# Performance work log

Measured on AMD Instinct MI355X. Metric: run time of the kernel, lower is better.

The kernel has to match this reference:

```python
import jax, jax.numpy as jnp
import numpy as np

L = 6
LVL = 2

def build_permutation_indices(L, l):
    delta = 4 ** (L - l - 1)
    tmp = np.tile(np.arange(4) * delta, delta)
    tmp += np.repeat(np.arange(delta), 4)
    tmp = np.tile(tmp, 4 ** l)
    tmp += np.repeat(np.arange(4 ** l) * 4 ** (L - l), 4 ** (L - l))
    return tmp.astype(np.int32)

def setup_inputs() -> dict:
    key = jax.random.key(0)
    ks = jax.random.split(key, 5)
    B, N, r = 16, 4 ** L, 32
    m, s = N // 4, 4 * r
    glorot = float(np.sqrt(1.0 / s))  # ~glorot scale for (s,s) matmul
    x = jax.random.normal(ks[0], (B, 2, N, r), dtype=jnp.float32)
    hr1 = jax.random.normal(ks[1], (m, s, s), dtype=jnp.float32) * glorot
    hi1 = jax.random.normal(ks[2], (m, s, s), dtype=jnp.float32) * glorot
    hr2 = jax.random.normal(ks[3], (m, s, s), dtype=jnp.float32) * glorot
    hi2 = jax.random.normal(ks[4], (m, s, s), dtype=jnp.float32) * glorot
    perm_idx = jnp.asarray(build_permutation_indices(L, LVL))
    return {"x": x, "hr1": hr1, "hi1": hi1, "hr2": hr2, "hi2": hi2, "perm_idx": perm_idx}

def reference(x, hr1, hi1, hr2, hi2, perm_idx):
    m = x.shape[-2] // 4
    s = x.shape[-1] * 4
    # permutation gather along the row axis, then regroup into m blocks of size s
    xp = jnp.take(x, perm_idx, axis=-2).reshape((-1, 2, m, s))
    x_re, x_im = xp[:, 0, :, :], xp[:, 1, :, :]
    # complex block-diagonal matmul: four real batched GEMMs over blocks 'a'
    y_re = jnp.einsum('baj,ajk->bak', x_re, hr1) + jnp.einsum('baj,ajk->bak', x_im, hi1)
    y_im = jnp.einsum('baj,ajk->bak', x_re, hi2) + jnp.einsum('baj,ajk->bak', x_im, hr2)
    y = jnp.stack([y_re, y_im], axis=1)
    n, r = m * 4, s // 4
    return y.reshape((-1, 2, n, r))
```

## Files before the change

kernel.cpp:

```cpp
#include <hip/hip_runtime.h>


__global__ __launch_bounds__(256, 4)
void hmat_kernel(const float* __restrict__ x,
                 const float* __restrict__ hr1,
                 const float* __restrict__ hi1,
                 const float* __restrict__ hr2,
                 const float* __restrict__ hi2,
                 const int* __restrict__ perm,
                 float* __restrict__ out) {
  __shared__ float lds[4096];
  const int a = blockIdx.x;
  const int t = threadIdx.x;

  {
    const int b    = t >> 4;
    const int c    = (t >> 3) & 1;
    const int jg   = (t >> 1) & 3;
    const int half = t & 1;
    const int row  = perm[a * 4 + jg];
    const float4* src =
        (const float4*)(x + ((size_t)(b * 2 + c) * 4096 + (size_t)row) * 32 +
                        half * 16);
#pragma unroll
    for (int q = 0; q < 4; ++q) {
      const float4 v = src[q];
      const int jb = jg * 32 + half * 16 + q * 4;
      lds[(jb + 0) * 32 + c * 16 + b] = v.x;
      lds[(jb + 1) * 32 + c * 16 + b] = v.y;
      lds[(jb + 2) * 32 + c * 16 + b] = v.z;
      lds[(jb + 3) * 32 + c * 16 + b] = v.w;
    }
  }
  __syncthreads();

  const int w    = t >> 6;
  const int ch   = w >> 1;
  const int jh   = w & 1;
  const int lane = t & 63;
  const int m    = lane >> 5;
  const int kg   = lane & 31;
  const int k0   = kg * 4;

  const float* __restrict__ Hm =
      (ch == 0) ? (m == 0 ? hr1 : hi1) : (m == 0 ? hi2 : hr2);
  const float* __restrict__ hp =
      Hm + (size_t)a * 16384 + (size_t)jh * 8192 + k0;
  const float* __restrict__ xp = lds + jh * 2048 + m * 16;

  float4 acc[16];
#pragma unroll
  for (int i = 0; i < 16; ++i) acc[i] = make_float4(0.f, 0.f, 0.f, 0.f);

  float4 pf0 = *(const float4*)(hp + 0 * 128);
  float4 pf1 = *(const float4*)(hp + 1 * 128);
  float4 pf2 = *(const float4*)(hp + 2 * 128);
  float4 pf3 = *(const float4*)(hp + 3 * 128);

#define CONSUME(PF, J)                                                     \
  {                                                                        \
    const float* xj = xp + (J) * 32;                                       \
    const float4 xa = *(const float4*)(xj + 0);                            \
    const float4 xb = *(const float4*)(xj + 4);                            \
    const float4 xc = *(const float4*)(xj + 8);                            \
    const float4 xd = *(const float4*)(xj + 12);                           \
    const float xs[16] = {xa.x, xa.y, xa.z, xa.w, xb.x, xb.y, xb.z, xb.w,  \
                          xc.x, xc.y, xc.z, xc.w, xd.x, xd.y, xd.z, xd.w}; \
    _Pragma("unroll") for (int bb = 0; bb < 16; ++bb) {                    \
      acc[bb].x = fmaf(xs[bb], (PF).x, acc[bb].x);                         \
      acc[bb].y = fmaf(xs[bb], (PF).y, acc[bb].y);                         \
      acc[bb].z = fmaf(xs[bb], (PF).z, acc[bb].z);                         \
      acc[bb].w = fmaf(xs[bb], (PF).w, acc[bb].w);                         \
    }                                                                      \
  }

  for (int j4 = 0; j4 < 60; j4 += 4) {
    CONSUME(pf0, j4 + 0); pf0 = *(const float4*)(hp + (j4 + 4) * 128);
    CONSUME(pf1, j4 + 1); pf1 = *(const float4*)(hp + (j4 + 5) * 128);
    CONSUME(pf2, j4 + 2); pf2 = *(const float4*)(hp + (j4 + 6) * 128);
    CONSUME(pf3, j4 + 3); pf3 = *(const float4*)(hp + (j4 + 7) * 128);
  }
  CONSUME(pf0, 60);
  CONSUME(pf1, 61);
  CONSUME(pf2, 62);
  CONSUME(pf3, 63);
#undef CONSUME

#pragma unroll
  for (int bb = 0; bb < 16; ++bb) {
    acc[bb].x += __shfl_xor(acc[bb].x, 32, 64);
    acc[bb].y += __shfl_xor(acc[bb].y, 32, 64);
    acc[bb].z += __shfl_xor(acc[bb].z, 32, 64);
    acc[bb].w += __shfl_xor(acc[bb].w, 32, 64);
  }

  __syncthreads();
  if (jh == 1 && m == 0) {
#pragma unroll
    for (int bb = 0; bb < 16; ++bb)
      *(float4*)&lds[ch * 2048 + bb * 128 + k0] = acc[bb];
  }
  __syncthreads();
  if (jh == 0 && m == 0) {
#pragma unroll
    for (int bb = 0; bb < 16; ++bb) {
      const float4 o = *(const float4*)&lds[ch * 2048 + bb * 128 + k0];
      float4 r;
      r.x = acc[bb].x + o.x;
      r.y = acc[bb].y + o.y;
      r.z = acc[bb].z + o.z;
      r.w = acc[bb].w + o.w;
      *(float4*)(out + (size_t)(bb * 2 + ch) * 131072 + (size_t)a * 128 + k0) =
          r;
    }
  }
}

extern "C" void kernel_launch(void* const* d_in, const int* in_sizes, int n_in,
                              void* d_out, int out_size, void* d_ws, size_t ws_size,
                              hipStream_t stream) {
  const float* x   = (const float*)d_in[0];
  const float* hr1 = (const float*)d_in[1];
  const float* hi1 = (const float*)d_in[2];
  const float* hr2 = (const float*)d_in[3];
  const float* hi2 = (const float*)d_in[4];
  const int* perm  = (const int*)d_in[5];
  float* out = (float*)d_out;

  hipLaunchKernelGGL(hmat_kernel, dim3(1024), dim3(256), 0, stream,
                     x, hr1, hi1, hr2, hi2, perm, out);
}
```

Measured before the change: 57.19 us.

## Swizzle LDS x tile, double-buffer LDS reads, and overlap H prefetch with staging

The x staging tile in LDS now uses an XOR swizzle on the column index, which is meant to cut bank conflicts on both the transposing writes and the float4 reads. The first H prefetch loads are issued before the barrier, so their global latency overlaps the x staging. LDS reads of x are double-buffered in registers one step ahead of the FMA block to hide LDS latency. The trade-off is more register pressure under launch_bounds(256,4), plus fiddly swizzle index arithmetic that must match between writes and reads.

```diff
diff --git a/kernel.cpp b/kernel.cpp
--- a/kernel.cpp
+++ b/kernel.cpp
@@ -13,27 +13,6 @@
   const int a = blockIdx.x;
   const int t = threadIdx.x;
 
-  {
-    const int b    = t >> 4;
-    const int c    = (t >> 3) & 1;
-    const int jg   = (t >> 1) & 3;
-    const int half = t & 1;
-    const int row  = perm[a * 4 + jg];
-    const float4* src =
-        (const float4*)(x + ((size_t)(b * 2 + c) * 4096 + (size_t)row) * 32 +
-                        half * 16);
-#pragma unroll
-    for (int q = 0; q < 4; ++q) {
-      const float4 v = src[q];
-      const int jb = jg * 32 + half * 16 + q * 4;
-      lds[(jb + 0) * 32 + c * 16 + b] = v.x;
-      lds[(jb + 1) * 32 + c * 16 + b] = v.y;
-      lds[(jb + 2) * 32 + c * 16 + b] = v.z;
-      lds[(jb + 3) * 32 + c * 16 + b] = v.w;
-    }
-  }
-  __syncthreads();
-
   const int w    = t >> 6;
   const int ch   = w >> 1;
   const int jh   = w & 1;
@@ -46,26 +25,55 @@
       (ch == 0) ? (m == 0 ? hr1 : hi1) : (m == 0 ? hi2 : hr2);
   const float* __restrict__ hp =
       Hm + (size_t)a * 16384 + (size_t)jh * 8192 + k0;
-  const float* __restrict__ xp = lds + jh * 2048 + m * 16;
 
-  float4 acc[16];
-#pragma unroll
-  for (int i = 0; i < 16; ++i) acc[i] = make_float4(0.f, 0.f, 0.f, 0.f);
+  {
+    const int b    = t >> 4;
+    const int c    = (t >> 3) & 1;
+    const int jg   = (t >> 1) & 3;
+    const int half = t & 1;
+    const int row  = perm[a * 4 + jg];
+    const float4* src =
+        (const float4*)(x + ((size_t)(b * 2 + c) * 4096 + (size_t)row) * 32 +
+                        half * 16);
+    float4 v0 = src[0], v1 = src[1], v2 = src[2], v3 = src[3];
+    const int col = (c * 16 + b) ^ ((((jg << 1) | half) & 3) << 2);
+    const int jb  = jg * 32 + half * 16;
+#define PUTX(V, Q)                             \
+  lds[(jb + (Q)*4 + 0) * 32 + col] = (V).x;    \
+  lds[(jb + (Q)*4 + 1) * 32 + col] = (V).y;    \
+  lds[(jb + (Q)*4 + 2) * 32 + col] = (V).z;    \
+  lds[(jb + (Q)*4 + 3) * 32 + col] = (V).w;
+    PUTX(v0, 0) PUTX(v1, 1) PUTX(v2, 2) PUTX(v3, 3)
+#undef PUTX
+  }
 
   float4 pf0 = *(const float4*)(hp + 0 * 128);
   float4 pf1 = *(const float4*)(hp + 1 * 128);
   float4 pf2 = *(const float4*)(hp + 2 * 128);
   float4 pf3 = *(const float4*)(hp + 3 * 128);
 
-#define CONSUME(PF, J)                                                     \
+  __syncthreads();
+
+  const float* __restrict__ xp = lds + m * 16;
+
+  float4 acc[16];
+#pragma unroll
+  for (int i = 0; i < 16; ++i) acc[i] = make_float4(0.f, 0.f, 0.f, 0.f);
+
+#define LOADX(X0, X1, X2, X3, J)                        \
+  {                                                     \
+    const float* xj = xp + (J) * 32;                    \
+    const int key = (((J) >> 4) & 3) << 2;              \
+    X0 = *(const float4*)(xj + (0 ^ key));              \
+    X1 = *(const float4*)(xj + (4 ^ key));              \
+    X2 = *(const float4*)(xj + (8 ^ key));              \
+    X3 = *(const float4*)(xj + (12 ^ key));             \
+  }
+
+#define CONSUME(PF, XA, XB, XC, XD)                                        \
   {                                                                        \
-    const float* xj = xp + (J) * 32;                                       \
-    const float4 xa = *(const float4*)(xj + 0);                            \
-    const float4 xb = *(const float4*)(xj + 4);                            \
-    const float4 xc = *(const float4*)(xj + 8);                            \
-    const float4 xd = *(const float4*)(xj + 12);                           \
-    const float xs[16] = {xa.x, xa.y, xa.z, xa.w, xb.x, xb.y, xb.z, xb.w,  \
-                          xc.x, xc.y, xc.z, xc.w, xd.x, xd.y, xd.z, xd.w}; \
+    const float xs[16] = {XA.x, XA.y, XA.z, XA.w, XB.x, XB.y, XB.z, XB.w,  \
+                          XC.x, XC.y, XC.z, XC.w, XD.x, XD.y, XD.z, XD.w}; \
     _Pragma("unroll") for (int bb = 0; bb < 16; ++bb) {                    \
       acc[bb].x = fmaf(xs[bb], (PF).x, acc[bb].x);                         \
       acc[bb].y = fmaf(xs[bb], (PF).y, acc[bb].y);                         \
@@ -74,16 +82,33 @@
     }                                                                      \
   }
 
+  const int jofs = jh * 64;
+
+  float4 xA0, xA1, xA2, xA3, xB0, xB1, xB2, xB3;
+  LOADX(xA0, xA1, xA2, xA3, jofs + 0)
+
   for (int j4 = 0; j4 < 60; j4 += 4) {
-    CONSUME(pf0, j4 + 0); pf0 = *(const float4*)(hp + (j4 + 4) * 128);
-    CONSUME(pf1, j4 + 1); pf1 = *(const float4*)(hp + (j4 + 5) * 128);
-    CONSUME(pf2, j4 + 2); pf2 = *(const float4*)(hp + (j4 + 6) * 128);
-    CONSUME(pf3, j4 + 3); pf3 = *(const float4*)(hp + (j4 + 7) * 128);
+    LOADX(xB0, xB1, xB2, xB3, jofs + j4 + 1)
+    CONSUME(pf0, xA0, xA1, xA2, xA3)
+    pf0 = *(const float4*)(hp + (j4 + 4) * 128);
+    LOADX(xA0, xA1, xA2, xA3, jofs + j4 + 2)
+    CONSUME(pf1, xB0, xB1, xB2, xB3)
+    pf1 = *(const float4*)(hp + (j4 + 5) * 128);
+    LOADX(xB0, xB1, xB2, xB3, jofs + j4 + 3)
+    CONSUME(pf2, xA0, xA1, xA2, xA3)
+    pf2 = *(const float4*)(hp + (j4 + 6) * 128);
+    LOADX(xA0, xA1, xA2, xA3, jofs + j4 + 4)
+    CONSUME(pf3, xB0, xB1, xB2, xB3)
+    pf3 = *(const float4*)(hp + (j4 + 7) * 128);
   }
-  CONSUME(pf0, 60);
-  CONSUME(pf1, 61);
-  CONSUME(pf2, 62);
-  CONSUME(pf3, 63);
+  LOADX(xB0, xB1, xB2, xB3, jofs + 61)
+  CONSUME(pf0, xA0, xA1, xA2, xA3)
+  LOADX(xA0, xA1, xA2, xA3, jofs + 62)
+  CONSUME(pf1, xB0, xB1, xB2, xB3)
+  LOADX(xB0, xB1, xB2, xB3, jofs + 63)
+  CONSUME(pf2, xA0, xA1, xA2, xA3)
+  CONSUME(pf3, xB0, xB1, xB2, xB3)
+#undef LOADX
 #undef CONSUME
 
 #pragma unroll
```

Result: slower. 104.3 us (+82.4%).

## Stream H weights into LDS ring buffer via async global_load_lds

Applied to the files above, without the earlier changes.

Replaces the four-deep register prefetch of H rows with a six-slot per-wave LDS ring filled by global_load_lds, gated by explicit vmcnt and lgkmcnt waits and sched barriers. It also remaps threads in the x gather and issues the H loads only after the x tile is staged. The intent is deeper latency hiding for the weight stream with fewer VGPRs. In exchange, LDS use grows from 16KB to 40KB per block, which can cut occupancy. Manual waitcnt handling is fragile, and the final steps re-issue clamped loads of row 63.

```diff
diff --git a/kernel.cpp b/kernel.cpp
--- a/kernel.cpp
+++ b/kernel.cpp
@@ -1,5 +1,12 @@
 #include <hip/hip_runtime.h>
 
+
+typedef unsigned int u32;
+__device__ __forceinline__ void gld_lds16(const float* g, float* l) {
+  __builtin_amdgcn_global_load_lds(
+      (const __attribute__((address_space(1))) u32*)g,
+      (__attribute__((address_space(3))) u32*)l, 16, 0, 0);
+}
 
 __global__ __launch_bounds__(256, 4)
 void hmat_kernel(const float* __restrict__ x,
@@ -9,30 +16,9 @@
                  const float* __restrict__ hi2,
                  const int* __restrict__ perm,
                  float* __restrict__ out) {
-  __shared__ float lds[4096];
+  __shared__ float lds[10240];
   const int a = blockIdx.x;
   const int t = threadIdx.x;
-
-  {
-    const int b    = t >> 4;
-    const int c    = (t >> 3) & 1;
-    const int jg   = (t >> 1) & 3;
-    const int half = t & 1;
-    const int row  = perm[a * 4 + jg];
-    const float4* src =
-        (const float4*)(x + ((size_t)(b * 2 + c) * 4096 + (size_t)row) * 32 +
-                        half * 16);
-#pragma unroll
-    for (int q = 0; q < 4; ++q) {
-      const float4 v = src[q];
-      const int jb = jg * 32 + half * 16 + q * 4;
-      lds[(jb + 0) * 32 + c * 16 + b] = v.x;
-      lds[(jb + 1) * 32 + c * 16 + b] = v.y;
-      lds[(jb + 2) * 32 + c * 16 + b] = v.z;
-      lds[(jb + 3) * 32 + c * 16 + b] = v.w;
-    }
-  }
-  __syncthreads();
 
   const int w    = t >> 6;
   const int ch   = w >> 1;
@@ -44,22 +30,52 @@
 
   const float* __restrict__ Hm =
       (ch == 0) ? (m == 0 ? hr1 : hi1) : (m == 0 ? hi2 : hr2);
-  const float* __restrict__ hp =
-      Hm + (size_t)a * 16384 + (size_t)jh * 8192 + k0;
-  const float* __restrict__ xp = lds + jh * 2048 + m * 16;
+  const float* __restrict__ hsrc = Hm + (size_t)a * 16384 + k0;
+  const int jofs = jh * 64;
+
+  {
+    const int c    = t & 1;
+    const int b    = (t >> 1) & 15;
+    const int q    = t >> 5;
+    const int jg   = q >> 1;
+    const int half = q & 1;
+    const int row  = perm[a * 4 + jg];
+    const float4* src =
+        (const float4*)(x + ((size_t)(b * 2 + c) * 4096 + (size_t)row) * 32 +
+                        half * 16);
+    float4 v0 = src[0], v1 = src[1], v2 = src[2], v3 = src[3];
+    const int col = c * 16 + b;
+    const int jb  = jg * 32 + half * 16;
+#define PUTX(V, Q)                            \
+  lds[(jb + (Q)*4 + 0) * 32 + col] = (V).x;   \
+  lds[(jb + (Q)*4 + 1) * 32 + col] = (V).y;   \
+  lds[(jb + (Q)*4 + 2) * 32 + col] = (V).z;   \
+  lds[(jb + (Q)*4 + 3) * 32 + col] = (V).w;
+    PUTX(v0, 0) PUTX(v1, 1) PUTX(v2, 2) PUTX(v3, 3)
+#undef PUTX
+  }
+
+  __syncthreads();
+
+  float* __restrict__ ring = &lds[4096 + w * 1536];
+
+#pragma unroll
+  for (int d = 0; d < 6; ++d)
+    gld_lds16(hsrc + (size_t)(jofs + d) * 128, ring + d * 256);
+
+  const float* __restrict__ xp = lds + m * 16;
 
   float4 acc[16];
 #pragma unroll
   for (int i = 0; i < 16; ++i) acc[i] = make_float4(0.f, 0.f, 0.f, 0.f);
 
-  float4 pf0 = *(const float4*)(hp + 0 * 128);
-  float4 pf1 = *(const float4*)(hp + 1 * 128);
-  float4 pf2 = *(const float4*)(hp + 2 * 128);
-  float4 pf3 = *(const float4*)(hp + 3 * 128);
-
-#define CONSUME(PF, J)                                                     \
+#define STEP(IB, S)                                                        \
   {                                                                        \
-    const float* xj = xp + (J) * 32;                                       \
+    const int i = (IB) + (S);                                              \
+    asm volatile("s_waitcnt vmcnt(5)" ::: "memory");                       \
+    __builtin_amdgcn_sched_barrier(0);                                     \
+    const float4 h = *(const float4*)(ring + (S) * 256 + lane * 4);        \
+    const float* xj = xp + (size_t)(jofs + i) * 32;                        \
     const float4 xa = *(const float4*)(xj + 0);                            \
     const float4 xb = *(const float4*)(xj + 4);                            \
     const float4 xc = *(const float4*)(xj + 8);                            \
@@ -67,24 +83,23 @@
     const float xs[16] = {xa.x, xa.y, xa.z, xa.w, xb.x, xb.y, xb.z, xb.w,  \
                           xc.x, xc.y, xc.z, xc.w, xd.x, xd.y, xd.z, xd.w}; \
     _Pragma("unroll") for (int bb = 0; bb < 16; ++bb) {                    \
-      acc[bb].x = fmaf(xs[bb], (PF).x, acc[bb].x);                         \
-      acc[bb].y = fmaf(xs[bb], (PF).y, acc[bb].y);                         \
-      acc[bb].z = fmaf(xs[bb], (PF).z, acc[bb].z);                         \
-      acc[bb].w = fmaf(xs[bb], (PF).w, acc[bb].w);                         \
+      acc[bb].x = fmaf(xs[bb], h.x, acc[bb].x);                            \
+      acc[bb].y = fmaf(xs[bb], h.y, acc[bb].y);                            \
+      acc[bb].z = fmaf(xs[bb], h.z, acc[bb].z);                            \
+      acc[bb].w = fmaf(xs[bb], h.w, acc[bb].w);                            \
     }                                                                      \
+    __builtin_amdgcn_sched_barrier(0);                                     \
+    asm volatile("s_waitcnt lgkmcnt(0)" ::: "memory");                     \
+    const int nr = (i + 6 > 63) ? 63 : (i + 6);                            \
+    gld_lds16(hsrc + (size_t)(jofs + nr) * 128, ring + (S) * 256);         \
   }
 
-  for (int j4 = 0; j4 < 60; j4 += 4) {
-    CONSUME(pf0, j4 + 0); pf0 = *(const float4*)(hp + (j4 + 4) * 128);
-    CONSUME(pf1, j4 + 1); pf1 = *(const float4*)(hp + (j4 + 5) * 128);
-    CONSUME(pf2, j4 + 2); pf2 = *(const float4*)(hp + (j4 + 6) * 128);
-    CONSUME(pf3, j4 + 3); pf3 = *(const float4*)(hp + (j4 + 7) * 128);
+  for (int ii = 0; ii < 60; ii += 6) {
+    STEP(ii, 0) STEP(ii, 1) STEP(ii, 2)
+    STEP(ii, 3) STEP(ii, 4) STEP(ii, 5)
   }
-  CONSUME(pf0, 60);
-  CONSUME(pf1, 61);
-  CONSUME(pf2, 62);
-  CONSUME(pf3, 63);
-#undef CONSUME
+  STEP(60, 0) STEP(60, 1) STEP(60, 2) STEP(60, 3)
+#undef STEP
 
 #pragma unroll
   for (int bb = 0; bb < 16; ++bb) {
```

Measured after the change: 135.6 us. 137% more time.
